# Optimization experiments

Hardware: AMD Instinct MI355X
Metric: run time of the kernel (lower is better)

Reference implementation:

```python
import jax, jax.numpy as jnp
import numpy as np

B, N, D = 1, 512, 128


def setup_inputs() -> dict:
    key = jax.random.key(0)
    ks = jax.random.split(key, 8)
    h = jax.random.normal(ks[0], (B, N, D), dtype=jnp.float32)
    rel_emb = jax.random.normal(ks[1], (B, N, N, D), dtype=jnp.float32)
    edge_mask = jax.random.bernoulli(ks[2], 0.5, (B, N, N))
    s2d = 1.0 / np.sqrt(2 * D)
    s1d = 1.0 / np.sqrt(D)
    return {
        "h": h,
        "rel_emb": rel_emb,
        "edge_mask": edge_mask,
        "msg_w1": jax.random.normal(ks[3], (2 * D, D), dtype=jnp.float32) * s2d,
        "msg_b1": jnp.zeros((D,), jnp.float32),
        "msg_w2": jax.random.normal(ks[4], (D, D), dtype=jnp.float32) * s1d,
        "msg_b2": jnp.zeros((D,), jnp.float32),
        "upd_w1": jax.random.normal(ks[5], (2 * D, D), dtype=jnp.float32) * s2d,
        "upd_b1": jnp.zeros((D,), jnp.float32),
        "upd_w2": jax.random.normal(ks[6], (D, D), dtype=jnp.float32) * s1d,
        "upd_b2": jnp.zeros((D,), jnp.float32),
        "ln_g": jnp.ones((D,), jnp.float32),
        "ln_b": jnp.zeros((D,), jnp.float32),
    }


def _layernorm(x, g, b, eps=1e-5):
    mu = x.mean(-1, keepdims=True)
    var = x.var(-1, keepdims=True)
    return (x - mu) * jax.lax.rsqrt(var + eps) * g + b


def reference(h, rel_emb, edge_mask, msg_w1, msg_b1, msg_w2, msg_b2,
              upd_w1, upd_b1, upd_w2, upd_b2, ln_g, ln_b):
    _, n, d = h.shape
    # msg_in = cat([h_j, e_ji]); h_j[b,i,j] = h[b,j], e_ji[b,i,j] = rel_emb[b,j,i]
    # Split first linear so the h-dependent part is computed once per sender j.
    w1_h, w1_e = msg_w1[:d], msg_w1[d:]
    hj_part = h @ w1_h                                   # [B,N,D], indexed by sender j
    e_ji = jnp.swapaxes(rel_emb, 1, 2)                   # [B,N(i),N(j),D]
    pre = hj_part[:, None, :, :] + jnp.einsum('bijd,de->bije', e_ji, w1_e) + msg_b1
    msgs = jax.nn.silu(pre) @ msg_w2 + msg_b2            # [B,N,N,D]
    mask = jnp.swapaxes(edge_mask, 1, 2).astype(h.dtype)  # [B,N(i),N(j)]
    agg = jnp.einsum('bijd,bij->bid', msgs, mask)        # masked sum over senders j
    upd_in = jnp.concatenate([h, agg], axis=-1)          # [B,N,2D]
    delta = jax.nn.silu(upd_in @ upd_w1 + upd_b1) @ upd_w2 + upd_b2
    return _layernorm(h + delta, ln_g, ln_b)
```

## Files before the change

### kernel.cpp

```cpp
#include <hip/hip_runtime.h>
#include <hip/hip_bf16.h>

#define NN 512
#define DD 128

typedef __bf16 bf16x8 __attribute__((ext_vector_type(8)));
typedef float f32x4 __attribute__((ext_vector_type(4)));

static __device__ __forceinline__ f32x4 mfma16(bf16x8 a, bf16x8 b, f32x4 c) {
  return __builtin_amdgcn_mfma_f32_16x16x32_bf16(a, b, c, 0, 0, 0);
}

__global__ void k_pre(const float* __restrict__ h,
                      const float* __restrict__ msg_w1,
                      const float* __restrict__ msg_b1,
                      const int* __restrict__ emask,
                      __bf16* __restrict__ w1t, float* __restrict__ hjp,
                      float* __restrict__ cnt) {
  __shared__ float hr[128];
  __shared__ int csum;
  int j = blockIdx.x, t = threadIdx.x;
  if (t == 0) csum = 0;
  hr[t] = h[j * 128 + t];
  __syncthreads();
  float a0 = msg_b1[t], a1 = 0.f;
  #pragma unroll 16
  for (int k = 0; k < 128; k += 2) {
    a0 += hr[k] * msg_w1[k * 128 + t];
    a1 += hr[k + 1] * msg_w1[(k + 1) * 128 + t];
  }
  hjp[j * 128 + t] = a0 + a1;
  if (t < 32) {
    int tt = j * 32 + t;
    int e = tt >> 7, k = tt & 127;
    w1t[e * 128 + k] = (__bf16)msg_w1[(128 + k) * 128 + e];
  }
  int s = 0;
  #pragma unroll
  for (int r = 0; r < 4; r++) s += emask[(t * 4 + r) * NN + j] ? 1 : 0;
  #pragma unroll
  for (int off = 32; off > 0; off >>= 1) s += __shfl_down(s, off, 64);
  if ((t & 63) == 0) atomicAdd(&csum, s);
  __syncthreads();
  if (t == 0) cnt[j] = (float)csum;
}

#define CVT(bf, xa, xb) { \
  bf[0] = (__bf16)xa[0]; bf[1] = (__bf16)xa[1]; \
  bf[2] = (__bf16)xa[2]; bf[3] = (__bf16)xa[3]; \
  bf[4] = (__bf16)xb[0]; bf[5] = (__bf16)xb[1]; \
  bf[6] = (__bf16)xb[2]; bf[7] = (__bf16)xb[3]; }

__global__ __launch_bounds__(256, 2) void k_main(
    const float* __restrict__ rel, const int* __restrict__ emask,
    const float* __restrict__ hjp, const __bf16* __restrict__ w1t_g,
    float* __restrict__ partial) {
  __shared__ __align__(16) __bf16 tile[2 * 16 * 136];
  __shared__ float mk[256];
  const int tid = threadIdx.x;
  const int wave = tid >> 6;
  const int lane = tid & 63;
  const int l15 = lane & 15;
  const int q = lane >> 4;

  const int it = blockIdx.x >> 5;
  const int jc = blockIdx.x & 31;
  const int irow = it * 16;
  const int jbase = jc * 16;

  mk[tid] = emask[(size_t)(jbase + (tid >> 4)) * NN + irow + (tid & 15)] ? 1.f : 0.f;

  bf16x8 aw00, aw01, aw02, aw03, aw10, aw11, aw12, aw13;
  {
    const __bf16* b0 = w1t_g + (wave * 32 + l15) * 128 + q * 8;
    aw00 = *(const bf16x8*)(b0);
    aw01 = *(const bf16x8*)(b0 + 32);
    aw02 = *(const bf16x8*)(b0 + 64);
    aw03 = *(const bf16x8*)(b0 + 96);
    const __bf16* b1 = b0 + 16 * 128;
    aw10 = *(const bf16x8*)(b1);
    aw11 = *(const bf16x8*)(b1 + 32);
    aw12 = *(const bf16x8*)(b1 + 64);
    aw13 = *(const bf16x8*)(b1 + 96);
  }

  f32x4 t0 = {0.f, 0.f, 0.f, 0.f}, t1 = t0;

  const int srow = tid >> 4;
  const int schunk = tid & 15;
  const float* sb = rel + ((size_t)jbase * NN + irow + srow) * DD + schunk * 8;
  __bf16* sd = tile + srow * 136 + schunk * 8;

  __syncthreads();

  f32x4 xa0 = {0.f, 0.f, 0.f, 0.f}, xb0 = xa0;
  f32x4 xa1 = xa0, xb1 = xa0;
  f32x4 xa2 = xa0, xb2 = xa0;
  f32x4 xa3 = xa0, xb3 = xa0;
  {
    f32x4 ra = xa0, rb = xa0;
    if (mk[srow] != 0.f) { ra = *(const f32x4*)sb; rb = *(const f32x4*)(sb + 4); }
    bf16x8 pub;
    CVT(pub, ra, rb)
    *(bf16x8*)sd = pub;
    if (mk[16 + srow] != 0.f) {
      const float* s = sb + (size_t)NN * DD;
      xa0 = *(const f32x4*)s; xb0 = *(const f32x4*)(s + 4);
    }
    if (mk[32 + srow] != 0.f) {
      const float* s = sb + 2 * (size_t)NN * DD;
      xa1 = *(const f32x4*)s; xb1 = *(const f32x4*)(s + 4);
    }
    if (mk[48 + srow] != 0.f) {
      const float* s = sb + 3 * (size_t)NN * DD;
      xa2 = *(const f32x4*)s; xb2 = *(const f32x4*)(s + 4);
    }
    if (mk[64 + srow] != 0.f) {
      const float* s = sb + 4 * (size_t)NN * DD;
      xa3 = *(const f32x4*)s; xb3 = *(const f32x4*)(s + 4);
    }
  }

  #define COMPUTE(JROW) { \
    const float ms = mk[(JROW) * 16 + l15]; \
    const __bf16* tp = tile + (((JROW) & 1) ? 2176 : 0) + l15 * 136 + q * 8; \
    bf16x8 bf0 = *(const bf16x8*)(tp); \
    bf16x8 bf1 = *(const bf16x8*)(tp + 32); \
    bf16x8 bf2 = *(const bf16x8*)(tp + 64); \
    bf16x8 bf3 = *(const bf16x8*)(tp + 96); \
    f32x4 p0 = {0.f, 0.f, 0.f, 0.f}, p1 = p0; \
    p0 = mfma16(aw00, bf0, p0); p1 = mfma16(aw10, bf0, p1); \
    p0 = mfma16(aw01, bf1, p0); p1 = mfma16(aw11, bf1, p1); \
    p0 = mfma16(aw02, bf2, p0); p1 = mfma16(aw12, bf2, p1); \
    p0 = mfma16(aw03, bf3, p0); p1 = mfma16(aw13, bf3, p1); \
    _Pragma("unroll") \
    for (int r = 0; r < 4; r++) { \
      float v0 = p0[r] + hv0[r]; \
      float v1 = p1[r] + hv1[r]; \
      t0[r] += ms * v0 * __builtin_amdgcn_rcpf(1.f + __expf(-v0)); \
      t1[r] += ms * v1 * __builtin_amdgcn_rcpf(1.f + __expf(-v1)); \
    } }

  #define STEP(JR, XA, XB) { \
    __syncthreads(); \
    const float* hjg = hjp + (size_t)(jbase + (JR)) * DD + wave * 32 + q * 4; \
    f32x4 hv0 = *(const f32x4*)(hjg); \
    f32x4 hv1 = *(const f32x4*)(hjg + 16); \
    if ((JR) + 1 < 16) { \
      bf16x8 pub; \
      CVT(pub, XA, XB) \
      *(bf16x8*)(sd + ((((JR) + 1) & 1) ? 2176 : 0)) = pub; \
    } \
    if ((JR) + 5 < 16) { \
      if (mk[((JR) + 5) * 16 + srow] != 0.f) { \
        const float* s = sb + (size_t)((JR) + 5) * NN * DD; \
        XA = *(const f32x4*)s; XB = *(const f32x4*)(s + 4); \
      } \
    } \
    COMPUTE(JR) }

  #pragma unroll 1
  for (int jj = 0; jj < 16; jj += 4) {
    STEP(jj,     xa0, xb0)
    STEP(jj + 1, xa1, xb1)
    STEP(jj + 2, xa2, xb2)
    STEP(jj + 3, xa3, xb3)
  }
  #undef STEP
  #undef COMPUTE

  float* pp = partial + ((size_t)jc * NN + irow + l15) * DD + wave * 32 + q * 4;
  *(f32x4*)pp = t0;
  *(f32x4*)(pp + 16) = t1;
}

__global__ void k_update(const float* __restrict__ h, const float* __restrict__ partial,
                         const float* __restrict__ w2, const float* __restrict__ b2,
                         const float* __restrict__ cnt,
                         const float* __restrict__ uw1, const float* __restrict__ ub1,
                         const float* __restrict__ uw2, const float* __restrict__ ub2,
                         const float* __restrict__ g, const float* __restrict__ bb,
                         float* __restrict__ out) {
  __shared__ float Trow[128];
  __shared__ float uin[256];
  __shared__ float zl[128];
  __shared__ float ss[4];
  int i = blockIdx.x, t = threadIdx.x;
  float hv = h[i * 128 + t];
  float ts = 0.f;
  #pragma unroll
  for (int c = 0; c < 32; c++) ts += partial[((size_t)c * NN + i) * DD + t];
  Trow[t] = ts;
  __syncthreads();
  float a0 = cnt[i] * b2[t], a1 = 0.f;
  #pragma unroll 16
  for (int e = 0; e < 128; e += 2) {
    a0 += Trow[e] * w2[e * 128 + t];
    a1 += Trow[e + 1] * w2[(e + 1) * 128 + t];
  }
  uin[t] = hv;
  uin[128 + t] = a0 + a1;
  __syncthreads();
  float z0 = ub1[t], z1 = 0.f, z2 = 0.f, z3 = 0.f;
  #pragma unroll 16
  for (int k = 0; k < 256; k += 4) {
    z0 += uin[k] * uw1[k * 128 + t];
    z1 += uin[k + 1] * uw1[(k + 1) * 128 + t];
    z2 += uin[k + 2] * uw1[(k + 2) * 128 + t];
    z3 += uin[k + 3] * uw1[(k + 3) * 128 + t];
  }
  float z = (z0 + z1) + (z2 + z3);
  z = z / (1.f + __expf(-z));
  zl[t] = z;
  __syncthreads();
  float d0 = ub2[t], d1 = 0.f;
  #pragma unroll 16
  for (int k = 0; k < 128; k += 2) {
    d0 += zl[k] * uw2[k * 128 + t];
    d1 += zl[k + 1] * uw2[(k + 1) * 128 + t];
  }
  float x = hv + d0 + d1;
  float s1 = x, s2 = x * x;
  #pragma unroll
  for (int off = 32; off > 0; off >>= 1) {
    s1 += __shfl_down(s1, off, 64);
    s2 += __shfl_down(s2, off, 64);
  }
  if ((t & 63) == 0) { ss[(t >> 6) * 2] = s1; ss[(t >> 6) * 2 + 1] = s2; }
  __syncthreads();
  s1 = ss[0] + ss[2];
  s2 = ss[1] + ss[3];
  float mu = s1 * (1.f / 128.f);
  float var = s2 * (1.f / 128.f) - mu * mu;
  out[i * 128 + t] = (x - mu) * rsqrtf(var + 1e-5f) * g[t] + bb[t];
}

extern "C" void kernel_launch(void* const* d_in, const int* in_sizes, int n_in,
                              void* d_out, int out_size, void* d_ws, size_t ws_size,
                              hipStream_t stream) {
  const float* h      = (const float*)d_in[0];
  const float* rel    = (const float*)d_in[1];
  const int*   emask  = (const int*)d_in[2];
  const float* msg_w1 = (const float*)d_in[3];
  const float* msg_b1 = (const float*)d_in[4];
  const float* msg_w2 = (const float*)d_in[5];
  const float* msg_b2 = (const float*)d_in[6];
  const float* upd_w1 = (const float*)d_in[7];
  const float* upd_b1 = (const float*)d_in[8];
  const float* upd_w2 = (const float*)d_in[9];
  const float* upd_b2 = (const float*)d_in[10];
  const float* ln_g   = (const float*)d_in[11];
  const float* ln_b   = (const float*)d_in[12];
  float* out = (float*)d_out;

  char* ws = (char*)d_ws;
  float*  hjp     = (float*)ws;
  __bf16* w1t     = (__bf16*)(ws + 262144);
  float*  cnt     = (float*)(ws + 262144 + 32768);
  float*  partial = (float*)(ws + 262144 + 36864);

  k_pre<<<512, 128, 0, stream>>>(h, msg_w1, msg_b1, emask, w1t, hjp, cnt);
  k_main<<<1024, 256, 0, stream>>>(rel, emask, hjp, w1t, partial);
  k_update<<<512, 128, 0, stream>>>(h, partial, msg_w2, msg_b2, cnt,
                                    upd_w1, upd_b1, upd_w2, upd_b2,
                                    ln_g, ln_b, out);
}
```

Baseline: 43.88 us.

## Load rel_emb fragments directly into registers per wave, dropping LDS staging and barriers

Replaces the shared-memory double-buffered bf16 tile with per-wave direct global loads of the MFMA B-operand fragments, converted to bf16 in registers, prefetching two j-rows ahead. The edge mask is kept as a per-lane bitmask in a register instead of an LDS array, which removes all __syncthreads. The aim is to cut barrier stalls and LDS traffic. In exchange, each of the four waves re-reads the same rel_emb data, raising global/L2 load traffic by four times, and register pressure grows.

```diff
diff --git a/kernel.cpp b/kernel.cpp
--- a/kernel.cpp
+++ b/kernel.cpp
@@ -55,8 +55,6 @@
     const float* __restrict__ rel, const int* __restrict__ emask,
     const float* __restrict__ hjp, const __bf16* __restrict__ w1t_g,
     float* __restrict__ partial) {
-  __shared__ __align__(16) __bf16 tile[2 * 16 * 136];
-  __shared__ float mk[256];
   const int tid = threadIdx.x;
   const int wave = tid >> 6;
   const int lane = tid & 63;
@@ -67,8 +65,6 @@
   const int jc = blockIdx.x & 31;
   const int irow = it * 16;
   const int jbase = jc * 16;
-
-  mk[tid] = emask[(size_t)(jbase + (tid >> 4)) * NN + irow + (tid & 15)] ? 1.f : 0.f;
 
   bf16x8 aw00, aw01, aw02, aw03, aw10, aw11, aw12, aw13;
   {
@@ -84,55 +80,45 @@
     aw13 = *(const bf16x8*)(b1 + 96);
   }
 
+  unsigned msk = 0;
+  #pragma unroll
+  for (int jr = 0; jr < 16; jr++)
+    msk |= (emask[(size_t)(jbase + jr) * NN + irow + l15] ? (1u << jr) : 0u);
+
   f32x4 t0 = {0.f, 0.f, 0.f, 0.f}, t1 = t0;
 
-  const int srow = tid >> 4;
-  const int schunk = tid & 15;
-  const float* sb = rel + ((size_t)jbase * NN + irow + srow) * DD + schunk * 8;
-  __bf16* sd = tile + srow * 136 + schunk * 8;
-
-  __syncthreads();
-
-  f32x4 xa0 = {0.f, 0.f, 0.f, 0.f}, xb0 = xa0;
-  f32x4 xa1 = xa0, xb1 = xa0;
-  f32x4 xa2 = xa0, xb2 = xa0;
-  f32x4 xa3 = xa0, xb3 = xa0;
-  {
-    f32x4 ra = xa0, rb = xa0;
-    if (mk[srow] != 0.f) { ra = *(const f32x4*)sb; rb = *(const f32x4*)(sb + 4); }
-    bf16x8 pub;
-    CVT(pub, ra, rb)
-    *(bf16x8*)sd = pub;
-    if (mk[16 + srow] != 0.f) {
-      const float* s = sb + (size_t)NN * DD;
-      xa0 = *(const f32x4*)s; xb0 = *(const f32x4*)(s + 4);
+  const float* rb = rel + ((size_t)jbase * NN + irow + l15) * DD + q * 8;
+
+  f32x4 X0 = {0.f, 0.f, 0.f, 0.f}, X1 = X0, X2 = X0, X3 = X0,
+        X4 = X0, X5 = X0, X6 = X0, X7 = X0;
+  f32x4 Y0 = X0, Y1 = X0, Y2 = X0, Y3 = X0,
+        Y4 = X0, Y5 = X0, Y6 = X0, Y7 = X0;
+
+  #define LOADSET(J, S0, S1, S2, S3, S4, S5, S6, S7) \
+    if ((msk >> (J)) & 1) { \
+      const float* s = rb + (size_t)(J) * (NN * DD); \
+      S0 = *(const f32x4*)(s);      S1 = *(const f32x4*)(s + 4); \
+      S2 = *(const f32x4*)(s + 32); S3 = *(const f32x4*)(s + 36); \
+      S4 = *(const f32x4*)(s + 64); S5 = *(const f32x4*)(s + 68); \
+      S6 = *(const f32x4*)(s + 96); S7 = *(const f32x4*)(s + 100); \
     }
-    if (mk[32 + srow] != 0.f) {
-      const float* s = sb + 2 * (size_t)NN * DD;
-      xa1 = *(const f32x4*)s; xb1 = *(const f32x4*)(s + 4);
-    }
-    if (mk[48 + srow] != 0.f) {
-      const float* s = sb + 3 * (size_t)NN * DD;
-      xa2 = *(const f32x4*)s; xb2 = *(const f32x4*)(s + 4);
-    }
-    if (mk[64 + srow] != 0.f) {
-      const float* s = sb + 4 * (size_t)NN * DD;
-      xa3 = *(const f32x4*)s; xb3 = *(const f32x4*)(s + 4);
-    }
-  }
-
-  #define COMPUTE(JROW) { \
-    const float ms = mk[(JROW) * 16 + l15]; \
-    const __bf16* tp = tile + (((JROW) & 1) ? 2176 : 0) + l15 * 136 + q * 8; \
-    bf16x8 bf0 = *(const bf16x8*)(tp); \
-    bf16x8 bf1 = *(const bf16x8*)(tp + 32); \
-    bf16x8 bf2 = *(const bf16x8*)(tp + 64); \
-    bf16x8 bf3 = *(const bf16x8*)(tp + 96); \
+
+  LOADSET(0, X0, X1, X2, X3, X4, X5, X6, X7)
+  LOADSET(1, Y0, Y1, Y2, Y3, Y4, Y5, Y6, Y7)
+
+  #define STEP(JR, S0, S1, S2, S3, S4, S5, S6, S7) { \
+    bf16x8 b0, b1, b2, b3; \
+    CVT(b0, S0, S1) CVT(b1, S2, S3) CVT(b2, S4, S5) CVT(b3, S6, S7) \
+    if ((JR) + 2 < 16) { LOADSET((JR) + 2, S0, S1, S2, S3, S4, S5, S6, S7) } \
+    const float ms = ((msk >> (JR)) & 1) ? 1.f : 0.f; \
+    const float* hjg = hjp + (size_t)(jbase + (JR)) * DD + wave * 32 + q * 4; \
+    f32x4 hv0 = *(const f32x4*)(hjg); \
+    f32x4 hv1 = *(const f32x4*)(hjg + 16); \
     f32x4 p0 = {0.f, 0.f, 0.f, 0.f}, p1 = p0; \
-    p0 = mfma16(aw00, bf0, p0); p1 = mfma16(aw10, bf0, p1); \
-    p0 = mfma16(aw01, bf1, p0); p1 = mfma16(aw11, bf1, p1); \
-    p0 = mfma16(aw02, bf2, p0); p1 = mfma16(aw12, bf2, p1); \
-    p0 = mfma16(aw03, bf3, p0); p1 = mfma16(aw13, bf3, p1); \
+    p0 = mfma16(aw00, b0, p0); p1 = mfma16(aw10, b0, p1); \
+    p0 = mfma16(aw01, b1, p0); p1 = mfma16(aw11, b1, p1); \
+    p0 = mfma16(aw02, b2, p0); p1 = mfma16(aw12, b2, p1); \
+    p0 = mfma16(aw03, b3, p0); p1 = mfma16(aw13, b3, p1); \
     _Pragma("unroll") \
     for (int r = 0; r < 4; r++) { \
       float v0 = p0[r] + hv0[r]; \
@@ -141,33 +127,13 @@
       t1[r] += ms * v1 * __builtin_amdgcn_rcpf(1.f + __expf(-v1)); \
     } }
 
-  #define STEP(JR, XA, XB) { \
-    __syncthreads(); \
-    const float* hjg = hjp + (size_t)(jbase + (JR)) * DD + wave * 32 + q * 4; \
-    f32x4 hv0 = *(const f32x4*)(hjg); \
-    f32x4 hv1 = *(const f32x4*)(hjg + 16); \
-    if ((JR) + 1 < 16) { \
-      bf16x8 pub; \
-      CVT(pub, XA, XB) \
-      *(bf16x8*)(sd + ((((JR) + 1) & 1) ? 2176 : 0)) = pub; \
-    } \
-    if ((JR) + 5 < 16) { \
-      if (mk[((JR) + 5) * 16 + srow] != 0.f) { \
-        const float* s = sb + (size_t)((JR) + 5) * NN * DD; \
-        XA = *(const f32x4*)s; XB = *(const f32x4*)(s + 4); \
-      } \
-    } \
-    COMPUTE(JR) }
-
   #pragma unroll 1
-  for (int jj = 0; jj < 16; jj += 4) {
-    STEP(jj,     xa0, xb0)
-    STEP(jj + 1, xa1, xb1)
-    STEP(jj + 2, xa2, xb2)
-    STEP(jj + 3, xa3, xb3)
+  for (int jj = 0; jj < 16; jj += 2) {
+    STEP(jj,     X0, X1, X2, X3, X4, X5, X6, X7)
+    STEP(jj + 1, Y0, Y1, Y2, Y3, Y4, Y5, Y6, Y7)
   }
   #undef STEP
-  #undef COMPUTE
+  #undef LOADSET
 
   float* pp = partial + ((size_t)jc * NN + irow + l15) * DD + wave * 32 + q * 4;
   *(f32x4*)pp = t0;
```

New measurement: 65.61 us. +49.5%, slower.
